# Optimization experiments

Measured on AMD Instinct MI355X. Metric: run time of the kernel, lower is better.

The kernel has to match this reference:

```python
import jax, jax.numpy as jnp
import numpy as np

B, K, D_MODEL = 4, 8400, 512
H, Q, V = 8, 64, 64
WIN, PAD = 168, 42
STEP = WIN - 2 * PAD  # 84


def setup_inputs() -> dict:
    key = jax.random.key(0)
    ks = jax.random.split(key, 11)
    s = 0.02
    return {
        "query": jax.random.normal(ks[0], (B, K, D_MODEL), jnp.float32),
        "key":   jax.random.normal(ks[1], (B, K, D_MODEL), jnp.float32),
        "value": jax.random.normal(ks[2], (B, K, D_MODEL), jnp.float32),
        "W_q": jax.random.normal(ks[3], (D_MODEL, Q * H), jnp.float32) * s,
        "b_q": jax.random.normal(ks[4], (Q * H,), jnp.float32) * s,
        "W_k": jax.random.normal(ks[5], (D_MODEL, Q * H), jnp.float32) * s,
        "b_k": jax.random.normal(ks[6], (Q * H,), jnp.float32) * s,
        "W_v": jax.random.normal(ks[7], (D_MODEL, V * H), jnp.float32) * s,
        "b_v": jax.random.normal(ks[8], (V * H,), jnp.float32) * s,
        "W_o": jax.random.normal(ks[9], (H * V, D_MODEL), jnp.float32) * s,
        "b_o": jax.random.normal(ks[10], (D_MODEL,), jnp.float32) * s,
    }


def _heads(x, d):
    # torch.cat(x.chunk(h, -1), dim=0): (B, Kp, h*d) -> (h*B, Kp, d), head-major
    b, kp, _ = x.shape
    return jnp.transpose(x.reshape(b, kp, H, d), (2, 0, 1, 3)).reshape(H * b, kp, d)


def reference(query, key, value, W_q, b_q, W_k, b_k, W_v, b_v, W_o, b_o):
    b = query.shape[0]
    # replicate padding along time axis
    pad = lambda x: jnp.pad(x, ((0, 0), (PAD, PAD), (0, 0)), mode="edge")
    qp, kp_, vp = pad(query), pad(key), pad(value)

    Qh = _heads(qp @ W_q + b_q, Q)   # (hB, Kp, Q)
    Kh = _heads(kp_ @ W_k + b_k, Q)
    Vh = _heads(vp @ W_v + b_v, V)

    n_win = K // STEP  # 100
    widx = jnp.arange(n_win)[:, None] * STEP + jnp.arange(WIN)[None, :]
    Qw = Qh[:, widx, :]
    Kw = Kh[:, widx, :]
    Vw = Vh[:, widx, :]

    scores = jnp.einsum("bnwq,bnxq->bnwx", Qw, Kw) / np.sqrt(WIN).astype(np.float32)
    tri = jnp.triu(jnp.ones((WIN, WIN), bool), 1)  # subsequent mask
    scores = jnp.where(tri, -jnp.inf, scores)
    attn_w = jax.nn.softmax(scores, axis=-1)
    attn = jnp.einsum("bnwx,bnxv->bnwv", attn_w, Vw)

    attn = attn[:, :, PAD:WIN - PAD, :]                      # crop padding
    attn = attn.reshape(H, b, n_win * STEP, V)               # (h, B, K, V)
    heads = jnp.transpose(attn, (1, 2, 0, 3)).reshape(b, K, H * V)
    return heads @ W_o + b_o
```

## Files before the change

### kernel.cpp

```cpp
#include <hip/hip_runtime.h>
#include <hip/hip_bf16.h>
#include <stdint.h>

#define BATCH 4
#define SEQ   8400
#define DM    512
#define KP    8484
#define NWIN  100
#define STEP_ 84
#define PAD_  42
#define NKEY  126
#define MROWS 33600
#define NTILES 266
#define TPB   13
#define NBI   21
#define OT_TPB 3
#define OT_NBI 350

typedef __attribute__((ext_vector_type(8))) short short8;
typedef __attribute__((ext_vector_type(4))) float float4v;
typedef __attribute__((ext_vector_type(4))) unsigned short ushort4v;

#define MFMA16 __builtin_amdgcn_mfma_f32_16x16x32_bf16

__device__ __forceinline__ unsigned short f2bf(float f) {
    union { float f; unsigned u; } v; v.f = f;
    return (unsigned short)((v.u + 0x7FFFu + ((v.u >> 16) & 1u)) >> 16);
}
__device__ __forceinline__ unsigned short bfc(float f) {
    __hip_bfloat16 h = __float2bfloat16(f);
    union { __hip_bfloat16 h; unsigned short u; } v; v.h = h;
    return v.u;
}

typedef __attribute__((address_space(1))) const unsigned int as1_cu32;
typedef __attribute__((address_space(3))) unsigned int as3_u32;
__device__ __forceinline__ void gload16(const void* g, void* l) {
    __builtin_amdgcn_global_load_lds((as1_cu32*)g, (as3_u32*)l, 16, 0, 0);
}

__global__ __launch_bounds__(256) void kprep(const float* __restrict__ Wq,
                                             const float* __restrict__ Wk,
                                             const float* __restrict__ Wv,
                                             const float* __restrict__ Wo,
                                             unsigned short* __restrict__ Wt) {
    const float* src = blockIdx.z == 0 ? Wq : blockIdx.z == 1 ? Wk
                     : blockIdx.z == 2 ? Wv : Wo;
    unsigned short* dst = Wt + (size_t)blockIdx.z * DM * DM;
    __shared__ float t[64][65];
    int c = threadIdx.x & 63, r4 = threadIdx.x >> 6;
    int kb = blockIdx.x * 64, nb = blockIdx.y * 64;
    for (int i = 0; i < 16; i++) {
        int r = r4 * 16 + i;
        t[r][c] = src[(size_t)(kb + r) * DM + nb + c];
    }
    __syncthreads();
    for (int i = 0; i < 16; i++) {
        int r = r4 * 16 + i;
        dst[(size_t)(nb + r) * DM + kb + c] = f2bf(t[c][r]);
    }
}

__global__ __launch_bounds__(512, 2) void kproj(const float* __restrict__ q,
                                                const float* __restrict__ k,
                                                const float* __restrict__ v,
                                                const unsigned short* __restrict__ Wt,
                                                const float* __restrict__ bq,
                                                const float* __restrict__ bk,
                                                const float* __restrict__ bv,
                                                unsigned short* __restrict__ Qb,
                                                unsigned short* __restrict__ Kb,
                                                unsigned short* __restrict__ VT) {
    int L = blockIdx.x;
    int P = (L >> 4) * 8 + (L & 7);
    int nhalf = (L >> 3) & 1;
    if (P >= 12 * NBI) return;
    int z = P / NBI, bi = P % NBI;
    int ten = z >> 2, b = z & 3;
    int t0 = bi * TPB;
    int tcnt = NTILES - t0; if (tcnt > TPB) tcnt = TPB;
    if (tcnt <= 0) return;

    const float* A = (ten == 0 ? q : ten == 1 ? k : v) + (size_t)b * SEQ * DM;
    const unsigned short* Wten = Wt + (size_t)ten * DM * DM;
    const float* bias = ten == 0 ? bq : ten == 1 ? bk : bv;
    float scale = ten == 0 ? 0.07715167498104595f : 1.f;

    __shared__ __align__(16) char lds[32768];

    int tid = threadIdx.x, lane = tid & 63, w = tid >> 6;
    int l15 = lane & 15, g = lane >> 4;
    int n0w = nhalf * 256 + w * 32;
    int h = n0w >> 6;
    int hb2 = h * BATCH + b;

    short8 Breg[2][16];
#pragma unroll
    for (int nf = 0; nf < 2; nf++)
#pragma unroll
        for (int s5 = 0; s5 < 16; s5++)
            Breg[nf][s5] = *(const short8*)(Wten +
                (size_t)(n0w + nf * 16 + l15) * DM + s5 * 32 + g * 8);

    float bias0 = bias[n0w + l15];
    float bias1 = bias[n0w + 16 + l15];

    int srow = tid >> 4, sc = tid & 15;
    int woff = srow * 1024 + ((sc ^ (srow & 7)) << 4);

    auto loadreg = [&](float4v (&d)[8], int tt) {
        int p = tt * 32 + srow; if (p > KP - 1) p = KP - 1;
        int ar = p - PAD_; ar = ar < 0 ? 0 : (ar > SEQ - 1 ? SEQ - 1 : ar);
        const float* s = A + (size_t)ar * DM + sc * 8;
#pragma unroll
        for (int j = 0; j < 4; j++) {
            d[2 * j]     = *(const float4v*)(s + j * 128);
            d[2 * j + 1] = *(const float4v*)(s + j * 128 + 4);
        }
    };

    float4v a[8];
    loadreg(a, t0);

    for (int ti = 0; ti < tcnt; ti++) {
        int tt = t0 + ti;
#pragma unroll
        for (int j = 0; j < 4; j++) {
            float4v f0 = a[2 * j], f1 = a[2 * j + 1];
            short8 h0;
            h0[0] = (short)bfc(f0.x); h0[1] = (short)bfc(f0.y);
            h0[2] = (short)bfc(f0.z); h0[3] = (short)bfc(f0.w);
            h0[4] = (short)bfc(f1.x); h0[5] = (short)bfc(f1.y);
            h0[6] = (short)bfc(f1.z); h0[7] = (short)bfc(f1.w);
            *(short8*)(lds + woff + j * 256) = h0;
        }
        if (ti + 1 < tcnt) loadreg(a, tt + 1);
        __builtin_amdgcn_sched_barrier(0);
        asm volatile("s_waitcnt lgkmcnt(0)" ::: "memory");
        __builtin_amdgcn_s_barrier();
        __builtin_amdgcn_sched_barrier(0);

        float4v acc[2][2];
#pragma unroll
        for (int mf = 0; mf < 2; mf++)
#pragma unroll
            for (int nf = 0; nf < 2; nf++) {
                float4v zz = {0.f, 0.f, 0.f, 0.f}; acc[mf][nf] = zz;
            }
#pragma unroll
        for (int s5 = 0; s5 < 16; s5++) {
            short8 afr[2];
#pragma unroll
            for (int mf = 0; mf < 2; mf++) {
                int row = mf * 16 + l15, c = s5 * 4 + g;
                afr[mf] = *(const short8*)(lds + row * 1024 + ((c ^ (row & 7)) << 4));
            }
#pragma unroll
            for (int mf = 0; mf < 2; mf++)
#pragma unroll
                for (int nf = 0; nf < 2; nf++)
                    acc[mf][nf] = MFMA16(afr[mf], Breg[nf][s5], acc[mf][nf], 0, 0, 0);
        }
        __builtin_amdgcn_s_barrier();
        __builtin_amdgcn_sched_barrier(0);

        int p0 = tt * 32;
        if (ten <= 1) {
            unsigned short* O = ten == 0 ? Qb : Kb;
#pragma unroll
            for (int nf = 0; nf < 2; nf++) {
                float bval = nf ? bias1 : bias0;
                int d = ((n0w + nf * 16) & 63) + l15;
                unsigned short* op = O + (size_t)hb2 * KP * 64 + d;
#pragma unroll
                for (int mf = 0; mf < 2; mf++) {
                    float4v vv = acc[mf][nf];
#pragma unroll
                    for (int r = 0; r < 4; r++) {
                        int p = p0 + mf * 16 + g * 4 + r;
                        if (p < KP)
                            op[(size_t)p * 64] = f2bf((vv[r] + bval) * scale);
                    }
                }
            }
        } else {
#pragma unroll
            for (int nf = 0; nf < 2; nf++) {
                float bval = nf ? bias1 : bias0;
                int d = ((n0w + nf * 16) & 63) + l15;
                unsigned short* base = VT + ((size_t)hb2 * 64 + d) * KP;
#pragma unroll
                for (int mf = 0; mf < 2; mf++) {
                    int p = p0 + mf * 16 + g * 4;
                    if (p <= KP - 4) {
                        float4v vv = acc[mf][nf];
                        ushort4v wv;
                        wv[0] = f2bf(vv.x + bval); wv[1] = f2bf(vv.y + bval);
                        wv[2] = f2bf(vv.z + bval); wv[3] = f2bf(vv.w + bval);
                        *(ushort4v*)(base + p) = wv;
                    }
                }
            }
        }
    }
}

__global__ __launch_bounds__(384) void kattn(const unsigned short* __restrict__ Qb,
                                             const unsigned short* __restrict__ Kb,
                                             const unsigned short* __restrict__ VT,
                                             unsigned short* __restrict__ attn) {
    int win = blockIdx.x, hb = blockIdx.y;
    int h = hb >> 2, b = hb & 3;
    const unsigned short* Qg = Qb + (size_t)hb * KP * 64;
    const unsigned short* Kg = Kb + (size_t)hb * KP * 64;
    const unsigned short* Vt = VT + (size_t)hb * 64 * KP;
    int p0 = win * STEP_;

    __shared__ __align__(16) char lds[45056];

    int tid = threadIdx.x, lane = tid & 63, f = tid >> 6;
    int l15 = lane & 15, g = lane >> 4;

#pragma unroll
    for (int it = 0; it < 5; it++) {
        int base = it * 384 + f * 64;
        if (base < 768) {
            int c = base + lane;
            int qi = c >> 3, kg = (c & 7) ^ (qi & 7);
            gload16(Qg + (size_t)(p0 + PAD_ + qi) * 64 + kg * 8, lds + base * 16);
        } else if (base < 1792) {
            int c = base + lane - 768;
            int x = c >> 3, kg = (c & 7) ^ (x & 7);
            gload16(Kg + (size_t)(p0 + x) * 64 + kg * 8, lds + base * 16);
        }
    }
    for (int c = tid; c < 2048; c += 384) {
        int d = c >> 5, c2 = c & 31;
        ushort4v wv = *(const ushort4v*)(Vt + (size_t)d * KP + p0 + c2 * 4);
        int cx = c2 >> 1;
        *(ushort4v*)(lds + 28672 + d * 256 + (((cx ^ (d & 7)) << 4) | ((c2 & 1) * 8))) = wv;
    }
    __syncthreads();

    short8 bq2[2];
    {
        int r = f * 16 + l15;
#pragma unroll
        for (int ks = 0; ks < 2; ks++) {
            int kg = ks * 4 + g;
            bq2[ks] = *(const short8*)(lds + r * 128 + ((kg ^ (r & 7)) << 4));
        }
    }
    float4v st[8];
#pragma unroll
    for (int xf = 0; xf < 8; xf++) {
        float4v zz = {0.f,0.f,0.f,0.f}; st[xf] = zz;
#pragma unroll
        for (int ks = 0; ks < 2; ks++) {
            int r = xf * 16 + l15;
            int kg = ks * 4 + g;
            short8 a = *(const short8*)(lds + 12288 + r * 128 + ((kg ^ (r & 7)) << 4));
            st[xf] = MFMA16(a, bq2[ks], st[xf], 0, 0, 0);
        }
    }

    int w_abs = PAD_ + f * 16 + l15;
    int w_eff = w_abs > 125 ? 125 : w_abs;
    float mx = -1e30f;
#pragma unroll
    for (int xf = 0; xf < 8; xf++)
#pragma unroll
        for (int r = 0; r < 4; r++) {
            int x = xf * 16 + g * 4 + r;
            float vv = st[xf][r];
            if (x > w_eff) vv = -1e30f;
            st[xf][r] = vv;
            mx = fmaxf(mx, vv);
        }
    mx = fmaxf(mx, __shfl_xor(mx, 16));
    mx = fmaxf(mx, __shfl_xor(mx, 32));
    float s = 0.f;
#pragma unroll
    for (int xf = 0; xf < 8; xf++)
#pragma unroll
        for (int r = 0; r < 4; r++) {
            float e = __expf(st[xf][r] - mx);
            st[xf][r] = e;
            s += e;
        }
    s += __shfl_xor(s, 16);
    s += __shfl_xor(s, 32);
    float inv = 1.f / s;

    __syncthreads();

    {
        int qi = f * 16 + l15;
#pragma unroll
        for (int xf = 0; xf < 8; xf++) {
            ushort4v pw;
#pragma unroll
            for (int r = 0; r < 4; r++) pw[r] = f2bf(st[xf][r] * inv);
            int xc = 2 * xf + (g >> 1);
            *(ushort4v*)(lds + qi * 256 + ((xc ^ (qi & 7)) << 4) + (g & 1) * 8) = pw;
        }
    }
    asm volatile("s_waitcnt lgkmcnt(0)" ::: "memory");
    __builtin_amdgcn_sched_barrier(0);

    float4v pv[4];
#pragma unroll
    for (int j = 0; j < 4; j++) { float4v zz = {0.f,0.f,0.f,0.f}; pv[j] = zz; }
    int qi = f * 16 + l15;
#pragma unroll
    for (int g2 = 0; g2 < 4; g2++) {
        int xc = g2 * 4 + g;
        short8 a = *(const short8*)(lds + qi * 256 + ((xc ^ (qi & 7)) << 4));
#pragma unroll
        for (int j = 0; j < 4; j++) {
            int d = j * 16 + l15;
            short8 bvv = *(const short8*)(lds + 28672 + d * 256 + ((xc ^ (d & 7)) << 4));
            pv[j] = MFMA16(a, bvv, pv[j], 0, 0, 0);
        }
    }

    __syncthreads();

    unsigned short* Ol = (unsigned short*)lds;
#pragma unroll
    for (int j = 0; j < 4; j++) {
        int d = j * 16 + l15;
#pragma unroll
        for (int r = 0; r < 4; r++) {
            int qq = f * 16 + g * 4 + r;
            int byte = qq * 128 + ((((d >> 3) ^ (qq & 7))) << 4) + (d & 7) * 2;
            *(unsigned short*)((char*)Ol + byte) = f2bf(pv[j][r]);
        }
    }
    __syncthreads();
    for (int c = tid; c < 672; c += 384) {
        int qq = c >> 3, ch = c & 7;
        short8 hv = *(const short8*)((char*)Ol + qq * 128 + ((ch ^ (qq & 7)) << 4));
        size_t off = ((size_t)(b * SEQ + win * STEP_ + qq) * DM) + h * 64 + ch * 8;
        *(short8*)(attn + off) = hv;
    }
}

__global__ __launch_bounds__(512, 2) void kout(const unsigned short* __restrict__ Ab,
                                               const unsigned short* __restrict__ W,
                                               const float* __restrict__ bias,
                                               float* __restrict__ Out) {
    int L = blockIdx.x;
    int P = (L >> 4) * 8 + (L & 7);
    int nhalf = (L >> 3) & 1;
    if (P >= OT_NBI) return;
    int t0 = P * OT_TPB;

    __shared__ __align__(16) char lds[32768];

    int tid = threadIdx.x, lane = tid & 63, w = tid >> 6;
    int l15 = lane & 15, g = lane >> 4;
    int n0w = nhalf * 256 + w * 32;

    short8 Breg[2][16];
#pragma unroll
    for (int nf = 0; nf < 2; nf++)
#pragma unroll
        for (int s5 = 0; s5 < 16; s5++)
            Breg[nf][s5] = *(const short8*)(W +
                (size_t)(n0w + nf * 16 + l15) * DM + s5 * 32 + g * 8);

    float bias0 = bias[n0w + l15];
    float bias1 = bias[n0w + 16 + l15];

    int srow = tid >> 4, sc = tid & 15;

    auto loadreg = [&](short8 (&d)[4], int tt) {
        const unsigned short* s = Ab + (size_t)(tt * 32 + srow) * DM;
#pragma unroll
        for (int j = 0; j < 4; j++)
            d[j] = *(const short8*)(s + (sc + j * 16) * 8);
    };

    short8 a[4];
    loadreg(a, t0);

    for (int ti = 0; ti < OT_TPB; ti++) {
        int tt = t0 + ti;
#pragma unroll
        for (int j = 0; j < 4; j++)
            *(short8*)(lds + srow * 1024 +
                       (((sc + j * 16) ^ (srow & 7)) << 4)) = a[j];
        if (ti + 1 < OT_TPB) loadreg(a, tt + 1);
        __builtin_amdgcn_sched_barrier(0);
        asm volatile("s_waitcnt lgkmcnt(0)" ::: "memory");
        __builtin_amdgcn_s_barrier();
        __builtin_amdgcn_sched_barrier(0);

        float4v acc[2][2];
#pragma unroll
        for (int mf = 0; mf < 2; mf++)
#pragma unroll
            for (int nf = 0; nf < 2; nf++) {
                float4v zz = {0.f, 0.f, 0.f, 0.f}; acc[mf][nf] = zz;
            }
#pragma unroll
        for (int s5 = 0; s5 < 16; s5++) {
            short8 afr[2];
#pragma unroll
            for (int mf = 0; mf < 2; mf++) {
                int row = mf * 16 + l15, c = s5 * 4 + g;
                afr[mf] = *(const short8*)(lds + row * 1024 + ((c ^ (row & 7)) << 4));
            }
#pragma unroll
            for (int mf = 0; mf < 2; mf++)
#pragma unroll
                for (int nf = 0; nf < 2; nf++)
                    acc[mf][nf] = MFMA16(afr[mf], Breg[nf][s5], acc[mf][nf], 0, 0, 0);
        }
        __builtin_amdgcn_s_barrier();
        __builtin_amdgcn_sched_barrier(0);

        int p0 = tt * 32;
#pragma unroll
        for (int nf = 0; nf < 2; nf++) {
            float bval = nf ? bias1 : bias0;
            int n = n0w + nf * 16 + l15;
#pragma unroll
            for (int mf = 0; mf < 2; mf++) {
                float4v vv = acc[mf][nf];
#pragma unroll
                for (int r = 0; r < 4; r++) {
                    int m = p0 + mf * 16 + g * 4 + r;
                    Out[(size_t)m * DM + n] = vv[r] + bval;
                }
            }
        }
    }
}

extern "C" void kernel_launch(void* const* d_in, const int* in_sizes, int n_in,
                              void* d_out, int out_size, void* d_ws, size_t ws_size,
                              hipStream_t stream) {
    const float* q  = (const float*)d_in[0];
    const float* k  = (const float*)d_in[1];
    const float* v  = (const float*)d_in[2];
    const float* Wq = (const float*)d_in[3];
    const float* bq = (const float*)d_in[4];
    const float* Wk = (const float*)d_in[5];
    const float* bk = (const float*)d_in[6];
    const float* Wv = (const float*)d_in[7];
    const float* bv = (const float*)d_in[8];
    const float* Wo = (const float*)d_in[9];
    const float* bo = (const float*)d_in[10];

    const size_t WT_ELEMS  = (size_t)4 * DM * DM;
    const size_t QKV_ELEMS = (size_t)32 * KP * 64;
    const size_t ATT_ELEMS = (size_t)MROWS * DM;
    size_t need = (WT_ELEMS + 3 * QKV_ELEMS + ATT_ELEMS) * 2;
    if (ws_size < need) return;

    unsigned short* Wt = (unsigned short*)d_ws;
    unsigned short* Qb = Wt + WT_ELEMS;
    unsigned short* Kb = Qb + QKV_ELEMS;
    unsigned short* VT = Kb + QKV_ELEMS;
    unsigned short* Ab = VT + QKV_ELEMS;

    kprep<<<dim3(8, 8, 4), dim3(256), 0, stream>>>(Wq, Wk, Wv, Wo, Wt);
    kproj<<<dim3(512), dim3(512), 0, stream>>>(q, k, v, Wt, bq, bk, bv,
                                               Qb, Kb, VT);
    kattn<<<dim3(NWIN, 32), dim3(384), 0, stream>>>(Qb, Kb, VT, Ab);
    kout<<<dim3(704), dim3(512), 0, stream>>>(Ab, Wt + 3 * DM * DM, bo,
                                              (float*)d_out);
}
```

Measured before the change: 187.1 us.

## Split projection N across four block groups and remap attention blocks across XCDs

The projection kernel now splits the 512 output columns into four groups of 128 instead of two halves of 256, so each wave holds one 16-column B fragment instead of two. This doubles the grid to 1024 blocks and raises the launch-bounds occupancy hint to 4 blocks per CU, aiming for more parallelism and latency hiding through lower register use. The cost is that each input A tile is loaded and converted twice as often. The attention kernel also remaps block ids so that consecutive windows of the same head/batch land on the same XCD, which should improve L2 reuse of the shared Q/K/V rows.

```diff
diff --git a/kernel.cpp b/kernel.cpp
--- a/kernel.cpp
+++ b/kernel.cpp
@@ -61,7 +61,7 @@
     }
 }
 
-__global__ __launch_bounds__(512, 2) void kproj(const float* __restrict__ q,
+__global__ __launch_bounds__(512, 4) void kproj(const float* __restrict__ q,
                                                 const float* __restrict__ k,
                                                 const float* __restrict__ v,
                                                 const unsigned short* __restrict__ Wt,
@@ -72,8 +72,8 @@
                                                 unsigned short* __restrict__ Kb,
                                                 unsigned short* __restrict__ VT) {
     int L = blockIdx.x;
-    int P = (L >> 4) * 8 + (L & 7);
-    int nhalf = (L >> 3) & 1;
+    int P = (L >> 5) * 8 + (L & 7);
+    int ngroup = (L >> 3) & 3;
     if (P >= 12 * NBI) return;
     int z = P / NBI, bi = P % NBI;
     int ten = z >> 2, b = z & 3;
@@ -90,20 +90,17 @@
 
     int tid = threadIdx.x, lane = tid & 63, w = tid >> 6;
     int l15 = lane & 15, g = lane >> 4;
-    int n0w = nhalf * 256 + w * 32;
+    int n0w = ngroup * 128 + w * 16;
     int h = n0w >> 6;
     int hb2 = h * BATCH + b;
 
-    short8 Breg[2][16];
-#pragma unroll
-    for (int nf = 0; nf < 2; nf++)
-#pragma unroll
-        for (int s5 = 0; s5 < 16; s5++)
-            Breg[nf][s5] = *(const short8*)(Wten +
-                (size_t)(n0w + nf * 16 + l15) * DM + s5 * 32 + g * 8);
+    short8 Breg[16];
+#pragma unroll
+    for (int s5 = 0; s5 < 16; s5++)
+        Breg[s5] = *(const short8*)(Wten +
+            (size_t)(n0w + l15) * DM + s5 * 32 + g * 8);
 
     float bias0 = bias[n0w + l15];
-    float bias1 = bias[n0w + 16 + l15];
 
     int srow = tid >> 4, sc = tid & 15;
     int woff = srow * 1024 + ((sc ^ (srow & 7)) << 4);
@@ -140,13 +137,11 @@
         __builtin_amdgcn_s_barrier();
         __builtin_amdgcn_sched_barrier(0);
 
-        float4v acc[2][2];
-#pragma unroll
-        for (int mf = 0; mf < 2; mf++)
-#pragma unroll
-            for (int nf = 0; nf < 2; nf++) {
-                float4v zz = {0.f, 0.f, 0.f, 0.f}; acc[mf][nf] = zz;
-            }
+        float4v acc[2];
+#pragma unroll
+        for (int mf = 0; mf < 2; mf++) {
+            float4v zz = {0.f, 0.f, 0.f, 0.f}; acc[mf] = zz;
+        }
 #pragma unroll
         for (int s5 = 0; s5 < 16; s5++) {
             short8 afr[2];
@@ -157,9 +152,7 @@
             }
 #pragma unroll
             for (int mf = 0; mf < 2; mf++)
-#pragma unroll
-                for (int nf = 0; nf < 2; nf++)
-                    acc[mf][nf] = MFMA16(afr[mf], Breg[nf][s5], acc[mf][nf], 0, 0, 0);
+                acc[mf] = MFMA16(afr[mf], Breg[s5], acc[mf], 0, 0, 0);
         }
         __builtin_amdgcn_s_barrier();
         __builtin_amdgcn_sched_barrier(0);
@@ -167,38 +160,30 @@
         int p0 = tt * 32;
         if (ten <= 1) {
             unsigned short* O = ten == 0 ? Qb : Kb;
-#pragma unroll
-            for (int nf = 0; nf < 2; nf++) {
-                float bval = nf ? bias1 : bias0;
-                int d = ((n0w + nf * 16) & 63) + l15;
-                unsigned short* op = O + (size_t)hb2 * KP * 64 + d;
-#pragma unroll
-                for (int mf = 0; mf < 2; mf++) {
-                    float4v vv = acc[mf][nf];
-#pragma unroll
-                    for (int r = 0; r < 4; r++) {
-                        int p = p0 + mf * 16 + g * 4 + r;
-                        if (p < KP)
-                            op[(size_t)p * 64] = f2bf((vv[r] + bval) * scale);
-                    }
+            int d = (n0w & 63) + l15;
+            unsigned short* op = O + (size_t)hb2 * KP * 64 + d;
+#pragma unroll
+            for (int mf = 0; mf < 2; mf++) {
+                float4v vv = acc[mf];
+#pragma unroll
+                for (int r = 0; r < 4; r++) {
+                    int p = p0 + mf * 16 + g * 4 + r;
+                    if (p < KP)
+                        op[(size_t)p * 64] = f2bf((vv[r] + bias0) * scale);
                 }
             }
         } else {
-#pragma unroll
-            for (int nf = 0; nf < 2; nf++) {
-                float bval = nf ? bias1 : bias0;
-                int d = ((n0w + nf * 16) & 63) + l15;
-                unsigned short* base = VT + ((size_t)hb2 * 64 + d) * KP;
-#pragma unroll
-                for (int mf = 0; mf < 2; mf++) {
-                    int p = p0 + mf * 16 + g * 4;
-                    if (p <= KP - 4) {
-                        float4v vv = acc[mf][nf];
-                        ushort4v wv;
-                        wv[0] = f2bf(vv.x + bval); wv[1] = f2bf(vv.y + bval);
-                        wv[2] = f2bf(vv.z + bval); wv[3] = f2bf(vv.w + bval);
-                        *(ushort4v*)(base + p) = wv;
-                    }
+            int d = (n0w & 63) + l15;
+            unsigned short* base = VT + ((size_t)hb2 * 64 + d) * KP;
+#pragma unroll
+            for (int mf = 0; mf < 2; mf++) {
+                int p = p0 + mf * 16 + g * 4;
+                if (p <= KP - 4) {
+                    float4v vv = acc[mf];
+                    ushort4v wv;
+                    wv[0] = f2bf(vv.x + bias0); wv[1] = f2bf(vv.y + bias0);
+                    wv[2] = f2bf(vv.z + bias0); wv[3] = f2bf(vv.w + bias0);
+                    *(ushort4v*)(base + p) = wv;
                 }
             }
         }
@@ -209,7 +194,9 @@
                                              const unsigned short* __restrict__ Kb,
                                              const unsigned short* __restrict__ VT,
                                              unsigned short* __restrict__ attn) {
-    int win = blockIdx.x, hb = blockIdx.y;
+    int nid = blockIdx.y * NWIN + blockIdx.x;
+    int work = (nid & 7) * 400 + (nid >> 3);
+    int win = work % NWIN, hb = work / NWIN;
     int h = hb >> 2, b = hb & 3;
     const unsigned short* Qg = Qb + (size_t)hb * KP * 64;
     const unsigned short* Kg = Kb + (size_t)hb * KP * 64;
@@ -467,8 +454,8 @@
     unsigned short* Ab = VT + QKV_ELEMS;
 
     kprep<<<dim3(8, 8, 4), dim3(256), 0, stream>>>(Wq, Wk, Wv, Wo, Wt);
-    kproj<<<dim3(512), dim3(512), 0, stream>>>(q, k, v, Wt, bq, bk, bv,
-                                               Qb, Kb, VT);
+    kproj<<<dim3(1024), dim3(512), 0, stream>>>(q, k, v, Wt, bq, bk, bv,
+                                                Qb, Kb, VT);
     kattn<<<dim3(NWIN, 32), dim3(384), 0, stream>>>(Qb, Kb, VT, Ab);
     kout<<<dim3(704), dim3(512), 0, stream>>>(Ab, Wt + 3 * DM * DM, bo,
                                               (float*)d_out);
```

Measured after the change: 267.9 us. 43.2% more time.
